# Kernel tuning notes

Hardware: AMD Instinct MI355X
Metric: run time of the kernel (lower is better)

## Reference

```python
import jax, jax.numpy as jnp
import numpy as np

H = 16
HIDDEN = 1024
B, S = 2, 2048


def setup_inputs() -> dict:
    key = jax.random.key(0)
    ks = jax.random.split(key, 6)
    return {
        "query": jax.random.normal(ks[0], (B, S, HIDDEN), dtype=jnp.float32),
        "key": jax.random.normal(ks[1], (B, S, HIDDEN), dtype=jnp.float32),
        "value": jax.random.normal(ks[2], (B, S, HIDDEN), dtype=jnp.float32),
        "W_query": jax.random.normal(ks[3], (HIDDEN, HIDDEN), dtype=jnp.float32) * 0.01,
        "W_key": jax.random.normal(ks[4], (HIDDEN, HIDDEN), dtype=jnp.float32) * 0.01,
        "W_value": jax.random.normal(ks[5], (HIDDEN, HIDDEN), dtype=jnp.float32) * 0.01,
        "ln_gamma": jnp.ones((HIDDEN,), dtype=jnp.float32),
        "ln_beta": jnp.zeros((HIDDEN,), dtype=jnp.float32),
        "mask": 1,
    }


def reference(query, key, value, W_query, W_key, W_value, ln_gamma, ln_beta, mask):
    b, s, hidden = query.shape
    d = hidden // H  # chunk_size per head
    # project then split last dim into heads, head axis leading: [h, b, s, d]
    def heads(x, W):
        return jnp.transpose((x @ W).reshape(b, s, H, d), (2, 0, 1, 3))
    q = heads(query, W_query)
    k = heads(key, W_key)
    v = heads(value, W_value)
    scale = jnp.asarray(np.sqrt(d), dtype=query.dtype)
    scores = jnp.einsum("hbqd,hbkd->hbqk", q, k) / scale
    aw = jax.nn.softmax(scores, axis=-1)
    if mask:
        tril = jnp.tril(jnp.ones((s, s), dtype=aw.dtype))  # post-softmax mask
        aw = aw * tril
        aw = aw / jnp.sum(aw, axis=3, keepdims=True)
    ws = jnp.einsum("hbqk,hbkd->hbqd", aw, v)
    # concat heads back on last dim: [b, s, hidden]
    ws = jnp.transpose(ws, (1, 2, 0, 3)).reshape(b, s, hidden)
    out = ws + query
    # LayerNorm over last dim, eps=1e-5 (torch default)
    mean = jnp.mean(out, axis=-1, keepdims=True)
    var = jnp.mean(jnp.square(out - mean), axis=-1, keepdims=True)
    out = (out - mean) / jnp.sqrt(var + 1e-5) * ln_gamma + ln_beta
    return out, aw
```

## Files before the change

### kernel.cpp

```cpp
#include <hip/hip_runtime.h>

typedef unsigned short ushort_t;
typedef __attribute__((ext_vector_type(4))) float f32x4;
typedef __attribute__((ext_vector_type(8))) short short8;
typedef __attribute__((ext_vector_type(8))) unsigned short ushort8;

#define B_DIM 2
#define S_LEN 2048
#define HID 1024
#define NH 16
#define HD 64
#define NROWS (B_DIM * S_LEN)

__device__ __forceinline__ ushort_t f2bf(float f) {
  union { float f; unsigned u; } v; v.f = f;
  unsigned r = v.u + 0x7FFFu + ((v.u >> 16) & 1u);
  return (ushort_t)(r >> 16);
}

__device__ __forceinline__ f32x4 zero4() {
  f32x4 z = {0.f, 0.f, 0.f, 0.f};
  return z;
}

struct WcArgs { const float* W[3]; ushort_t* T[3]; };

__global__ __launch_bounds__(256) void wconv_kernel(WcArgs args) {
  __shared__ ushort_t L[64 * 65];
  const int k0 = blockIdx.x * 64, n0 = blockIdx.y * 64;
  const float* __restrict__ W = args.W[blockIdx.z];
  ushort_t* __restrict__ T = args.T[blockIdx.z];
  const int tid = threadIdx.x;
  for (int i = 0; i < 4; ++i) {
    int idx = i * 256 + tid;
    int row = idx >> 4;
    int f4  = idx & 15;
    f32x4 v = *(const f32x4*)(W + (size_t)(k0 + row) * HID + n0 + f4 * 4);
    for (int j = 0; j < 4; ++j)
      L[(f4 * 4 + j) * 65 + row] = f2bf(v[j]);
  }
  __syncthreads();
  for (int i = 0; i < 2; ++i) {
    int idx = i * 256 + tid;
    int row = idx >> 3;
    int seg = idx & 7;
    ushort8 u;
    for (int j = 0; j < 8; ++j) u[j] = L[row * 65 + seg * 8 + j];
    *(ushort8*)(T + (size_t)(n0 + row) * HID + k0 + seg * 8) = u;
  }
}

struct PgArgs { const float* A[3]; const ushort_t* Wt[3]; ushort_t* C[3]; };

__global__ __launch_bounds__(256) void proj_gemm(PgArgs args) {
  __shared__ ushort_t As[128 * 64];
  __shared__ ushort_t Bs[128 * 64];
  const int z = blockIdx.z;
  const float* __restrict__ A = args.A[z];
  const ushort_t* __restrict__ Wt = args.Wt[z];
  ushort_t* __restrict__ C = args.C[z];
  const int tid = threadIdx.x;
  const int w = tid >> 6, lane = tid & 63, g = lane >> 4, c = lane & 15;
  const int wm = w >> 1, wn = w & 1;
  const int m0 = blockIdx.y * 128, n0 = blockIdx.x * 128;
  const int swz = (c & 7) << 3;

  f32x4 acc[4][4];
  for (int mi = 0; mi < 4; ++mi)
    for (int ni = 0; ni < 4; ++ni) acc[mi][ni] = zero4();

  for (int kt = 0; kt < 16; ++kt) {
    const int k0 = kt * 64;
    __syncthreads();
    for (int i = 0; i < 4; ++i) {
      int idx = i * 256 + tid;
      int row = idx >> 3, seg = idx & 7;
      const float* src = A + (size_t)(m0 + row) * HID + k0 + seg * 8;
      f32x4 a0 = *(const f32x4*)src;
      f32x4 a1 = *(const f32x4*)(src + 4);
      ushort8 u;
      u[0] = f2bf(a0[0]); u[1] = f2bf(a0[1]); u[2] = f2bf(a0[2]); u[3] = f2bf(a0[3]);
      u[4] = f2bf(a1[0]); u[5] = f2bf(a1[1]); u[6] = f2bf(a1[2]); u[7] = f2bf(a1[3]);
      *(ushort8*)&As[row * 64 + ((seg * 8) ^ ((row & 7) << 3))] = u;
    }
    for (int i = 0; i < 4; ++i) {
      int idx = i * 256 + tid;
      int row = idx >> 3, seg = idx & 7;
      ushort8 u = *(const ushort8*)(Wt + (size_t)(n0 + row) * HID + k0 + seg * 8);
      *(ushort8*)&Bs[row * 64 + ((seg * 8) ^ ((row & 7) << 3))] = u;
    }
    __syncthreads();
    for (int ks = 0; ks < 2; ++ks) {
      short8 af[4], bf4[4];
      for (int mi = 0; mi < 4; ++mi)
        af[mi] = *(const short8*)&As[(wm * 64 + mi * 16 + c) * 64 + ((ks * 32 + 8 * g) ^ swz)];
      for (int ni = 0; ni < 4; ++ni)
        bf4[ni] = *(const short8*)&Bs[(wn * 64 + ni * 16 + c) * 64 + ((ks * 32 + 8 * g) ^ swz)];
      for (int mi = 0; mi < 4; ++mi)
        for (int ni = 0; ni < 4; ++ni)
          acc[mi][ni] = __builtin_amdgcn_mfma_f32_16x16x32_bf16(af[mi], bf4[ni], acc[mi][ni], 0, 0, 0);
    }
  }
  for (int mi = 0; mi < 4; ++mi)
    for (int ni = 0; ni < 4; ++ni)
      for (int r = 0; r < 4; ++r)
        C[(size_t)(m0 + wm * 64 + mi * 16 + 4 * g + r) * HID + n0 + wn * 64 + ni * 16 + c] =
            f2bf(acc[mi][ni][r]);
}

__global__ __launch_bounds__(256) void attn_kernel(const ushort_t* __restrict__ Qb,
    const ushort_t* __restrict__ Kb, const ushort_t* __restrict__ Vb,
    float* __restrict__ aw, float* __restrict__ wsa) {
  __shared__ ushort_t Ks[64 * 64];
  __shared__ ushort_t Vt[64 * 64];
  __shared__ ushort_t Ps[4 * 16 * 64];

  const int tid = threadIdx.x;
  const int w = tid >> 6, lane = tid & 63, g = lane >> 4, c = lane & 15;
  const int qt = blockIdx.x, hb = blockIdx.y;
  const int h = hb >> 1, b = hb & 1;
  const int q0 = qt * 64;
  const int swz = (c & 7) << 3;
  const float C2 = 0.18033688011112042f;

  short8 aq[2];
  {
    const ushort_t* qp = Qb + (size_t)(b * S_LEN + q0 + w * 16 + c) * HID + h * HD + 8 * g;
    aq[0] = *(const short8*)qp;
    aq[1] = *(const short8*)(qp + 32);
  }

  float rs[4] = {0.f, 0.f, 0.f, 0.f};

  for (int kt = 0; kt <= qt; ++kt) {
    const int kc0 = kt * 64;
    __syncthreads();
    for (int i = 0; i < 2; ++i) {
      int idx = i * 256 + tid;
      int kk = idx >> 3, seg = idx & 7;
      const ushort_t* src = Kb + (size_t)(b * S_LEN + kc0 + kk) * HID + h * HD + seg * 8;
      *(ushort8*)&Ks[kk * 64 + ((seg * 8) ^ ((kk & 7) << 3))] = *(const ushort8*)src;
    }
    __syncthreads();
    f32x4 sf[4];
    for (int nf = 0; nf < 4; ++nf) sf[nf] = zero4();
    for (int ks = 0; ks < 2; ++ks) {
      short8 bk[4];
      for (int nf = 0; nf < 4; ++nf)
        bk[nf] = *(const short8*)&Ks[(nf * 16 + c) * 64 + ((ks * 32 + 8 * g) ^ swz)];
      for (int nf = 0; nf < 4; ++nf)
        sf[nf] = __builtin_amdgcn_mfma_f32_16x16x32_bf16(aq[ks], bk[nf], sf[nf], 0, 0, 0);
    }
    if (kt == qt) {
      for (int nf = 0; nf < 4; ++nf)
        for (int r = 0; r < 4; ++r)
          rs[r] += (nf * 16 + c > w * 16 + 4 * g + r) ? 0.f : exp2f(sf[nf][r] * C2);
    } else {
      for (int nf = 0; nf < 4; ++nf)
        for (int r = 0; r < 4; ++r) rs[r] += exp2f(sf[nf][r] * C2);
    }
  }
  for (int m = 1; m <= 8; m <<= 1)
    for (int r = 0; r < 4; ++r) rs[r] += __shfl_xor(rs[r], m);
  float linv[4];
  for (int r = 0; r < 4; ++r) linv[r] = 1.0f / rs[r];

  f32x4 oacc[4];
  for (int nf = 0; nf < 4; ++nf) oacc[nf] = zero4();

  for (int kt = 0; kt <= qt; ++kt) {
    const int kc0 = kt * 64;
    __syncthreads();
    for (int i = 0; i < 2; ++i) {
      int idx = i * 256 + tid;
      int kk = idx >> 3, seg = idx & 7;
      const ushort_t* src = Kb + (size_t)(b * S_LEN + kc0 + kk) * HID + h * HD + seg * 8;
      *(ushort8*)&Ks[kk * 64 + ((seg * 8) ^ ((kk & 7) << 3))] = *(const ushort8*)src;
    }
    for (int i = 0; i < 2; ++i) {
      int idx = i * 256 + tid;
      int dd = idx & 63, kseg = idx >> 6;
      ushort8 tv;
      for (int j = 0; j < 8; ++j)
        tv[j] = Vb[(size_t)(b * S_LEN + kc0 + kseg * 8 + j) * HID + h * HD + dd];
      *(ushort8*)&Vt[dd * 64 + ((kseg * 8) ^ ((dd & 7) << 3))] = tv;
    }
    __syncthreads();
    f32x4 sf[4];
    for (int nf = 0; nf < 4; ++nf) sf[nf] = zero4();
    for (int ks = 0; ks < 2; ++ks) {
      short8 bk[4];
      for (int nf = 0; nf < 4; ++nf)
        bk[nf] = *(const short8*)&Ks[(nf * 16 + c) * 64 + ((ks * 32 + 8 * g) ^ swz)];
      for (int nf = 0; nf < 4; ++nf)
        sf[nf] = __builtin_amdgcn_mfma_f32_16x16x32_bf16(aq[ks], bk[nf], sf[nf], 0, 0, 0);
    }
    const bool diag = (kt == qt);
    for (int nf = 0; nf < 4; ++nf) {
      for (int r = 0; r < 4; ++r) {
        float p = exp2f(sf[nf][r] * C2) * linv[r];
        if (diag && (nf * 16 + c > w * 16 + 4 * g + r)) p = 0.f;
        const int r16 = 4 * g + r;
        aw[((size_t)hb * S_LEN + q0 + w * 16 + r16) * S_LEN + kc0 + nf * 16 + c] = p;
        Ps[w * 1024 + r16 * 64 + ((nf * 16 + c) ^ ((r16 & 7) << 3))] = f2bf(p);
      }
    }
    for (int ks = 0; ks < 2; ++ks) {
      short8 pa = *(const short8*)&Ps[w * 1024 + c * 64 + ((ks * 32 + 8 * g) ^ swz)];
      short8 bv[4];
      for (int nf = 0; nf < 4; ++nf)
        bv[nf] = *(const short8*)&Vt[(nf * 16 + c) * 64 + ((ks * 32 + 8 * g) ^ swz)];
      for (int nf = 0; nf < 4; ++nf)
        oacc[nf] = __builtin_amdgcn_mfma_f32_16x16x32_bf16(pa, bv[nf], oacc[nf], 0, 0, 0);
    }
  }

  for (int nf = 0; nf < 4; ++nf)
    for (int r = 0; r < 4; ++r)
      wsa[(size_t)(b * S_LEN + q0 + w * 16 + 4 * g + r) * HID + h * HD + nf * 16 + c] =
          oacc[nf][r];

  const int z0 = (qt + 1) * 64;
  if (z0 < S_LEN) {
    const int row = tid >> 2, t4 = tid & 3;
    f32x4* rowp = (f32x4*)(aw + ((size_t)hb * S_LEN + q0 + row) * S_LEN);
    const f32x4 zz = zero4();
    for (int c4 = (z0 >> 2) + t4; c4 < (S_LEN >> 2); c4 += 4) rowp[c4] = zz;
  }
}

__global__ __launch_bounds__(256) void ln_kernel(const float* __restrict__ wsa,
    const float* __restrict__ qin, const float* __restrict__ gamma,
    const float* __restrict__ beta, float* __restrict__ out) {
  __shared__ float red[8];
  const int row = blockIdx.x, tid = threadIdx.x;
  const size_t base = (size_t)row * HID + tid * 4;
  f32x4 xv = *(const f32x4*)(wsa + base);
  f32x4 qv = *(const f32x4*)(qin + base);
  f32x4 x = xv + qv;
  float s = x[0] + x[1] + x[2] + x[3];
  float sq = x[0] * x[0] + x[1] * x[1] + x[2] * x[2] + x[3] * x[3];
  for (int m = 1; m <= 32; m <<= 1) {
    s += __shfl_xor(s, m);
    sq += __shfl_xor(sq, m);
  }
  if ((tid & 63) == 0) {
    red[(tid >> 6) * 2] = s;
    red[(tid >> 6) * 2 + 1] = sq;
  }
  __syncthreads();
  s = red[0] + red[2] + red[4] + red[6];
  sq = red[1] + red[3] + red[5] + red[7];
  const float mean = s * (1.0f / HID);
  const float var = sq * (1.0f / HID) - mean * mean;
  const float rstd = 1.0f / sqrtf(var + 1e-5f);
  f32x4 gm = *(const f32x4*)(gamma + tid * 4);
  f32x4 bt = *(const f32x4*)(beta + tid * 4);
  f32x4 o;
  for (int j = 0; j < 4; ++j) o[j] = (x[j] - mean) * rstd * gm[j] + bt[j];
  *(f32x4*)(out + base) = o;
}

extern "C" void kernel_launch(void* const* d_in, const int* in_sizes, int n_in,
                              void* d_out, int out_size, void* d_ws, size_t ws_size,
                              hipStream_t stream) {
  (void)in_sizes; (void)n_in; (void)out_size; (void)ws_size;
  const float* q_in = (const float*)d_in[0];
  const float* k_in = (const float*)d_in[1];
  const float* v_in = (const float*)d_in[2];
  const float* wq   = (const float*)d_in[3];
  const float* wk   = (const float*)d_in[4];
  const float* wv   = (const float*)d_in[5];
  const float* gamma = (const float*)d_in[6];
  const float* beta  = (const float*)d_in[7];

  ushort_t* base = (ushort_t*)d_ws;
  ushort_t* Wt0 = base;
  ushort_t* Wt1 = Wt0 + 1048576;
  ushort_t* Wt2 = Wt1 + 1048576;
  ushort_t* Qb = Wt2 + 1048576;
  ushort_t* Kb = Qb + 4194304;
  ushort_t* Vb = Kb + 4194304;
  float* wsa = (float*)(Vb + 4194304);

  float* out = (float*)d_out;
  float* aw = out + (size_t)NROWS * HID;

  WcArgs wc{{wq, wk, wv}, {Wt0, Wt1, Wt2}};
  wconv_kernel<<<dim3(16, 16, 3), 256, 0, stream>>>(wc);

  PgArgs pg{{q_in, k_in, v_in}, {Wt0, Wt1, Wt2}, {Qb, Kb, Vb}};
  proj_gemm<<<dim3(8, 32, 3), 256, 0, stream>>>(pg);

  attn_kernel<<<dim3(32, 32), 256, 0, stream>>>(Qb, Kb, Vb, aw, wsa);

  ln_kernel<<<dim3(NROWS), 256, 0, stream>>>(wsa, q_in, gamma, beta, out);
}
```

Before: 809.7 us.

## Pair causal query tiles per block, pre-transpose V, prefetch K/V, bf16 attention output

The attention kernel now gives each block a low and a high query tile (p and 31-p), which balances the causal work and lets both tiles share each loaded K/V tile. A separate kernel pre-transposes V so attention loads it with vector reads instead of strided scalar gathers. K/V tiles for the next step are prefetched into registers while the current one is computed, and QK^T is computed transposed so aw rows can be stored as vectors. The attention output is also stored as bf16 to cut LN input traffic, at some accuracy cost and with an extra kernel launch and more register pressure.

```diff
diff --git a/kernel.cpp b/kernel.cpp
--- a/kernel.cpp
+++ b/kernel.cpp
@@ -2,6 +2,7 @@
 
 typedef unsigned short ushort_t;
 typedef __attribute__((ext_vector_type(4))) float f32x4;
+typedef __attribute__((ext_vector_type(4))) unsigned short u16x4;
 typedef __attribute__((ext_vector_type(8))) short short8;
 typedef __attribute__((ext_vector_type(8))) unsigned short ushort8;
 
@@ -18,9 +19,21 @@
   return (ushort_t)(r >> 16);
 }
 
+__device__ __forceinline__ float bf2f(ushort_t h) {
+  union { unsigned u; float f; } v;
+  v.u = ((unsigned)h) << 16;
+  return v.f;
+}
+
 __device__ __forceinline__ f32x4 zero4() {
   f32x4 z = {0.f, 0.f, 0.f, 0.f};
   return z;
+}
+
+__device__ __forceinline__ unsigned pk2(float a, float b) {
+  unsigned r;
+  asm("v_cvt_pk_bf16_f32 %0, %1, %2" : "=v"(r) : "v"(a), "v"(b));
+  return r;
 }
 
 struct WcArgs { const float* W[3]; ushort_t* T[3]; };
@@ -108,136 +121,246 @@
             f2bf(acc[mi][ni][r]);
 }
 
+__global__ __launch_bounds__(256) void vtrans_kernel(const ushort_t* __restrict__ Vb,
+                                                     ushort_t* __restrict__ VT) {
+  __shared__ ushort_t L[64 * 72];
+  const int s0 = blockIdx.x * 64, hb = blockIdx.y;
+  const int h = hb >> 1, b = hb & 1;
+  const int tid = threadIdx.x;
+#pragma unroll
+  for (int i = 0; i < 2; ++i) {
+    int idx = i * 256 + tid;
+    int sr = idx >> 3, seg = idx & 7;
+    ushort8 u = *(const ushort8*)(Vb + ((size_t)(b * S_LEN) + s0 + sr) * HID + h * HD + seg * 8);
+    *(ushort8*)&L[sr * 72 + seg * 8] = u;
+  }
+  __syncthreads();
+#pragma unroll
+  for (int i = 0; i < 2; ++i) {
+    int idx = i * 256 + tid;
+    int d = idx >> 3, seg2 = idx & 7;
+    ushort8 u;
+#pragma unroll
+    for (int j = 0; j < 8; ++j) u[j] = L[(seg2 * 8 + j) * 72 + d];
+    *(ushort8*)(VT + ((size_t)hb * HD + d) * S_LEN + s0 + seg2 * 8) = u;
+  }
+}
+
+#define C2S 0.18033688011112042f
+
+__device__ __forceinline__ void qkt_tile(const ushort_t* Ks, int g, int c,
+                                         const short8 qB[2], f32x4 st[4]) {
+#pragma unroll
+  for (int nf = 0; nf < 4; ++nf) st[nf] = zero4();
+#pragma unroll
+  for (int ks = 0; ks < 2; ++ks) {
+#pragma unroll
+    for (int nf = 0; nf < 4; ++nf) {
+      short8 kf = *(const short8*)&Ks[(nf * 16 + c) * 64 + 8 * ((4 * ks + g) ^ (c & 7))];
+      st[nf] = __builtin_amdgcn_mfma_f32_16x16x32_bf16(kf, qB[ks], st[nf], 0, 0, 0);
+    }
+  }
+}
+
+__device__ __forceinline__ float tile_sum(const f32x4 st[4], int g, int c, int wq, bool diag) {
+  float s = 0.f;
+#pragma unroll
+  for (int nf = 0; nf < 4; ++nf)
+#pragma unroll
+    for (int r = 0; r < 4; ++r) {
+      float e = exp2f(st[nf][r] * C2S);
+      bool m = diag && (nf * 16 + 4 * g + r > wq);
+      s += m ? 0.f : e;
+    }
+  return s;
+}
+
+__device__ __forceinline__ void tile_p_pv(const f32x4 st[4], float linv, int g, int c,
+                                          bool diag, int wq, float* __restrict__ awrow,
+                                          char* psb, const short8 vf[2][4], f32x4 oacc[4]) {
+#pragma unroll
+  for (int nf = 0; nf < 4; ++nf) {
+    f32x4 pv;
+#pragma unroll
+    for (int r = 0; r < 4; ++r) {
+      float e = exp2f(st[nf][r] * C2S) * linv;
+      bool m = diag && (nf * 16 + 4 * g + r > wq);
+      pv[r] = m ? 0.f : e;
+    }
+    *(f32x4*)(awrow + nf * 16 + 4 * g) = pv;
+    uint2 u;
+    u.x = pk2(pv[0], pv[1]);
+    u.y = pk2(pv[2], pv[3]);
+    *(uint2*)(psb + (c * 128 + ((32 * nf + 8 * g) ^ ((c & 7) << 4)))) = u;
+  }
+#pragma unroll
+  for (int ks = 0; ks < 2; ++ks) {
+    short8 pf = *(const short8*)(psb + (c * 128 + ((64 * ks + 16 * g) ^ ((c & 7) << 4))));
+#pragma unroll
+    for (int nf = 0; nf < 4; ++nf)
+      oacc[nf] = __builtin_amdgcn_mfma_f32_16x16x32_bf16(vf[ks][nf], pf, oacc[nf], 0, 0, 0);
+  }
+}
+
 __global__ __launch_bounds__(256) void attn_kernel(const ushort_t* __restrict__ Qb,
-    const ushort_t* __restrict__ Kb, const ushort_t* __restrict__ Vb,
-    float* __restrict__ aw, float* __restrict__ wsa) {
+    const ushort_t* __restrict__ Kb, const ushort_t* __restrict__ VT,
+    float* __restrict__ aw, ushort_t* __restrict__ wsa) {
   __shared__ ushort_t Ks[64 * 64];
   __shared__ ushort_t Vt[64 * 64];
   __shared__ ushort_t Ps[4 * 16 * 64];
 
   const int tid = threadIdx.x;
   const int w = tid >> 6, lane = tid & 63, g = lane >> 4, c = lane & 15;
-  const int qt = blockIdx.x, hb = blockIdx.y;
+  const int p = blockIdx.x, hb = blockIdx.y;
   const int h = hb >> 1, b = hb & 1;
-  const int q0 = qt * 64;
-  const int swz = (c & 7) << 3;
-  const float C2 = 0.18033688011112042f;
-
-  short8 aq[2];
+  const int lo = p, hi = 31 - p;
+  const int wq = w * 16 + c;
+  const int srow = tid >> 3, sseg = tid & 7;
+
+  short8 qlo[2], qhi[2];
   {
-    const ushort_t* qp = Qb + (size_t)(b * S_LEN + q0 + w * 16 + c) * HID + h * HD + 8 * g;
-    aq[0] = *(const short8*)qp;
-    aq[1] = *(const short8*)(qp + 32);
-  }
-
-  float rs[4] = {0.f, 0.f, 0.f, 0.f};
-
-  for (int kt = 0; kt <= qt; ++kt) {
+    const ushort_t* qp = Qb + ((size_t)(b * S_LEN) + lo * 64 + wq) * HID + h * HD + 8 * g;
+    qlo[0] = *(const short8*)qp;
+    qlo[1] = *(const short8*)(qp + 32);
+    const ushort_t* qp2 = Qb + ((size_t)(b * S_LEN) + hi * 64 + wq) * HID + h * HD + 8 * g;
+    qhi[0] = *(const short8*)qp2;
+    qhi[1] = *(const short8*)(qp2 + 32);
+  }
+
+  ushort8 kr[2], vr[2], kn[2], vn[2];
+
+#pragma unroll
+  for (int i = 0; i < 2; ++i) {
+    int row = i * 32 + srow;
+    kr[i] = *(const ushort8*)(Kb + ((size_t)(b * S_LEN) + row) * HID + h * HD + sseg * 8);
+  }
+#pragma unroll
+  for (int i = 0; i < 2; ++i) {
+    int row = i * 32 + srow;
+    *(ushort8*)&Ks[row * 64 + 8 * (sseg ^ (row & 7))] = kr[i];
+  }
+  __syncthreads();
+
+  float ps_lo = 0.f, ps_hi = 0.f;
+  for (int kt = 0; kt <= hi; ++kt) {
+    if (kt < hi) {
+#pragma unroll
+      for (int i = 0; i < 2; ++i) {
+        int row = i * 32 + srow;
+        kn[i] = *(const ushort8*)(Kb + ((size_t)(b * S_LEN) + (kt + 1) * 64 + row) * HID + h * HD + sseg * 8);
+      }
+    }
+    f32x4 st[4];
+    qkt_tile(Ks, g, c, qhi, st);
+    ps_hi += tile_sum(st, g, c, wq, kt == hi);
+    if (kt <= lo) {
+      qkt_tile(Ks, g, c, qlo, st);
+      ps_lo += tile_sum(st, g, c, wq, kt == lo);
+    }
+    __syncthreads();
+    if (kt < hi) {
+#pragma unroll
+      for (int i = 0; i < 2; ++i) {
+        int row = i * 32 + srow;
+        *(ushort8*)&Ks[row * 64 + 8 * (sseg ^ (row & 7))] = kn[i];
+      }
+    }
+    __syncthreads();
+  }
+  ps_lo += __shfl_xor(ps_lo, 16); ps_lo += __shfl_xor(ps_lo, 32);
+  ps_hi += __shfl_xor(ps_hi, 16); ps_hi += __shfl_xor(ps_hi, 32);
+  const float linv_lo = 1.0f / ps_lo, linv_hi = 1.0f / ps_hi;
+
+  f32x4 oLo[4], oHi[4];
+#pragma unroll
+  for (int nf = 0; nf < 4; ++nf) { oLo[nf] = zero4(); oHi[nf] = zero4(); }
+
+#pragma unroll
+  for (int i = 0; i < 2; ++i) {
+    int row = i * 32 + srow;
+    kr[i] = *(const ushort8*)(Kb + ((size_t)(b * S_LEN) + row) * HID + h * HD + sseg * 8);
+    vr[i] = *(const ushort8*)(VT + ((size_t)hb * HD + row) * S_LEN + sseg * 8);
+  }
+#pragma unroll
+  for (int i = 0; i < 2; ++i) {
+    int row = i * 32 + srow;
+    *(ushort8*)&Ks[row * 64 + 8 * (sseg ^ (row & 7))] = kr[i];
+    *(ushort8*)&Vt[row * 64 + 8 * (sseg ^ (row & 7))] = vr[i];
+  }
+  __syncthreads();
+
+  char* psb = (char*)Ps + w * 2048;
+  for (int kt = 0; kt <= hi; ++kt) {
     const int kc0 = kt * 64;
-    __syncthreads();
-    for (int i = 0; i < 2; ++i) {
-      int idx = i * 256 + tid;
-      int kk = idx >> 3, seg = idx & 7;
-      const ushort_t* src = Kb + (size_t)(b * S_LEN + kc0 + kk) * HID + h * HD + seg * 8;
-      *(ushort8*)&Ks[kk * 64 + ((seg * 8) ^ ((kk & 7) << 3))] = *(const ushort8*)src;
-    }
-    __syncthreads();
-    f32x4 sf[4];
-    for (int nf = 0; nf < 4; ++nf) sf[nf] = zero4();
-    for (int ks = 0; ks < 2; ++ks) {
-      short8 bk[4];
+    if (kt < hi) {
+#pragma unroll
+      for (int i = 0; i < 2; ++i) {
+        int row = i * 32 + srow;
+        kn[i] = *(const ushort8*)(Kb + ((size_t)(b * S_LEN) + kc0 + 64 + row) * HID + h * HD + sseg * 8);
+        vn[i] = *(const ushort8*)(VT + ((size_t)hb * HD + row) * S_LEN + kc0 + 64 + sseg * 8);
+      }
+    }
+    short8 vf[2][4];
+#pragma unroll
+    for (int ks = 0; ks < 2; ++ks)
+#pragma unroll
       for (int nf = 0; nf < 4; ++nf)
-        bk[nf] = *(const short8*)&Ks[(nf * 16 + c) * 64 + ((ks * 32 + 8 * g) ^ swz)];
-      for (int nf = 0; nf < 4; ++nf)
-        sf[nf] = __builtin_amdgcn_mfma_f32_16x16x32_bf16(aq[ks], bk[nf], sf[nf], 0, 0, 0);
-    }
-    if (kt == qt) {
-      for (int nf = 0; nf < 4; ++nf)
-        for (int r = 0; r < 4; ++r)
-          rs[r] += (nf * 16 + c > w * 16 + 4 * g + r) ? 0.f : exp2f(sf[nf][r] * C2);
-    } else {
-      for (int nf = 0; nf < 4; ++nf)
-        for (int r = 0; r < 4; ++r) rs[r] += exp2f(sf[nf][r] * C2);
-    }
-  }
-  for (int m = 1; m <= 8; m <<= 1)
-    for (int r = 0; r < 4; ++r) rs[r] += __shfl_xor(rs[r], m);
-  float linv[4];
-  for (int r = 0; r < 4; ++r) linv[r] = 1.0f / rs[r];
-
-  f32x4 oacc[4];
-  for (int nf = 0; nf < 4; ++nf) oacc[nf] = zero4();
-
-  for (int kt = 0; kt <= qt; ++kt) {
-    const int kc0 = kt * 64;
-    __syncthreads();
-    for (int i = 0; i < 2; ++i) {
-      int idx = i * 256 + tid;
-      int kk = idx >> 3, seg = idx & 7;
-      const ushort_t* src = Kb + (size_t)(b * S_LEN + kc0 + kk) * HID + h * HD + seg * 8;
-      *(ushort8*)&Ks[kk * 64 + ((seg * 8) ^ ((kk & 7) << 3))] = *(const ushort8*)src;
-    }
-    for (int i = 0; i < 2; ++i) {
-      int idx = i * 256 + tid;
-      int dd = idx & 63, kseg = idx >> 6;
-      ushort8 tv;
-      for (int j = 0; j < 8; ++j)
-        tv[j] = Vb[(size_t)(b * S_LEN + kc0 + kseg * 8 + j) * HID + h * HD + dd];
-      *(ushort8*)&Vt[dd * 64 + ((kseg * 8) ^ ((dd & 7) << 3))] = tv;
-    }
-    __syncthreads();
-    f32x4 sf[4];
-    for (int nf = 0; nf < 4; ++nf) sf[nf] = zero4();
-    for (int ks = 0; ks < 2; ++ks) {
-      short8 bk[4];
-      for (int nf = 0; nf < 4; ++nf)
-        bk[nf] = *(const short8*)&Ks[(nf * 16 + c) * 64 + ((ks * 32 + 8 * g) ^ swz)];
-      for (int nf = 0; nf < 4; ++nf)
-        sf[nf] = __builtin_amdgcn_mfma_f32_16x16x32_bf16(aq[ks], bk[nf], sf[nf], 0, 0, 0);
-    }
-    const bool diag = (kt == qt);
-    for (int nf = 0; nf < 4; ++nf) {
-      for (int r = 0; r < 4; ++r) {
-        float p = exp2f(sf[nf][r] * C2) * linv[r];
-        if (diag && (nf * 16 + c > w * 16 + 4 * g + r)) p = 0.f;
-        const int r16 = 4 * g + r;
-        aw[((size_t)hb * S_LEN + q0 + w * 16 + r16) * S_LEN + kc0 + nf * 16 + c] = p;
-        Ps[w * 1024 + r16 * 64 + ((nf * 16 + c) ^ ((r16 & 7) << 3))] = f2bf(p);
+        vf[ks][nf] = *(const short8*)&Vt[(nf * 16 + c) * 64 + 8 * ((4 * ks + g) ^ (c & 7))];
+
+    f32x4 st[4];
+    qkt_tile(Ks, g, c, qhi, st);
+    {
+      float* awrow = aw + ((size_t)hb * S_LEN + hi * 64 + wq) * S_LEN + kc0;
+      tile_p_pv(st, linv_hi, g, c, kt == hi, wq, awrow, psb, vf, oHi);
+    }
+    if (kt <= lo) {
+      qkt_tile(Ks, g, c, qlo, st);
+      float* awrow = aw + ((size_t)hb * S_LEN + lo * 64 + wq) * S_LEN + kc0;
+      tile_p_pv(st, linv_lo, g, c, kt == lo, wq, awrow, psb, vf, oLo);
+    }
+    __syncthreads();
+    if (kt < hi) {
+#pragma unroll
+      for (int i = 0; i < 2; ++i) {
+        int row = i * 32 + srow;
+        *(ushort8*)&Ks[row * 64 + 8 * (sseg ^ (row & 7))] = kn[i];
+        *(ushort8*)&Vt[row * 64 + 8 * (sseg ^ (row & 7))] = vn[i];
       }
     }
-    for (int ks = 0; ks < 2; ++ks) {
-      short8 pa = *(const short8*)&Ps[w * 1024 + c * 64 + ((ks * 32 + 8 * g) ^ swz)];
-      short8 bv[4];
-      for (int nf = 0; nf < 4; ++nf)
-        bv[nf] = *(const short8*)&Vt[(nf * 16 + c) * 64 + ((ks * 32 + 8 * g) ^ swz)];
-      for (int nf = 0; nf < 4; ++nf)
-        oacc[nf] = __builtin_amdgcn_mfma_f32_16x16x32_bf16(pa, bv[nf], oacc[nf], 0, 0, 0);
-    }
-  }
-
-  for (int nf = 0; nf < 4; ++nf)
-    for (int r = 0; r < 4; ++r)
-      wsa[(size_t)(b * S_LEN + q0 + w * 16 + 4 * g + r) * HID + h * HD + nf * 16 + c] =
-          oacc[nf][r];
-
-  const int z0 = (qt + 1) * 64;
-  if (z0 < S_LEN) {
-    const int row = tid >> 2, t4 = tid & 3;
-    f32x4* rowp = (f32x4*)(aw + ((size_t)hb * S_LEN + q0 + row) * S_LEN);
-    const f32x4 zz = zero4();
-    for (int c4 = (z0 >> 2) + t4; c4 < (S_LEN >> 2); c4 += 4) rowp[c4] = zz;
-  }
-}
-
-__global__ __launch_bounds__(256) void ln_kernel(const float* __restrict__ wsa,
+    __syncthreads();
+  }
+
+#pragma unroll
+  for (int nf = 0; nf < 4; ++nf) {
+    uint2 uh, ul;
+    uh.x = pk2(oHi[nf][0], oHi[nf][1]); uh.y = pk2(oHi[nf][2], oHi[nf][3]);
+    ul.x = pk2(oLo[nf][0], oLo[nf][1]); ul.y = pk2(oLo[nf][2], oLo[nf][3]);
+    *(uint2*)(wsa + ((size_t)(b * S_LEN) + hi * 64 + wq) * HID + h * HD + nf * 16 + 4 * g) = uh;
+    *(uint2*)(wsa + ((size_t)(b * S_LEN) + lo * 64 + wq) * HID + h * HD + nf * 16 + 4 * g) = ul;
+  }
+
+  const f32x4 zz = zero4();
+#pragma unroll
+  for (int t = 0; t < 2; ++t) {
+    const int tIdx = t ? hi : lo;
+    const int z0q = (tIdx + 1) * 16;
+    for (int rr = 0; rr < 16; ++rr) {
+      f32x4* rowp = (f32x4*)(aw + ((size_t)hb * S_LEN + tIdx * 64 + w * 16 + rr) * S_LEN);
+      for (int c4 = z0q + lane; c4 < 512; c4 += 64) rowp[c4] = zz;
+    }
+  }
+}
+
+__global__ __launch_bounds__(256) void ln_kernel(const ushort_t* __restrict__ wsa,
     const float* __restrict__ qin, const float* __restrict__ gamma,
     const float* __restrict__ beta, float* __restrict__ out) {
   __shared__ float red[8];
   const int row = blockIdx.x, tid = threadIdx.x;
   const size_t base = (size_t)row * HID + tid * 4;
-  f32x4 xv = *(const f32x4*)(wsa + base);
+  u16x4 xh = *(const u16x4*)(wsa + base);
   f32x4 qv = *(const f32x4*)(qin + base);
-  f32x4 x = xv + qv;
+  f32x4 x;
+  for (int j = 0; j < 4; ++j) x[j] = bf2f(xh[j]) + qv[j];
   float s = x[0] + x[1] + x[2] + x[3];
   float sq = x[0] * x[0] + x[1] * x[1] + x[2] * x[2] + x[3] * x[3];
   for (int m = 1; m <= 32; m <<= 1) {
@@ -281,7 +404,8 @@
   ushort_t* Qb = Wt2 + 1048576;
   ushort_t* Kb = Qb + 4194304;
   ushort_t* Vb = Kb + 4194304;
-  float* wsa = (float*)(Vb + 4194304);
+  ushort_t* VT = Vb + 4194304;
+  ushort_t* wsa = VT + 4194304;
 
   float* out = (float*)d_out;
   float* aw = out + (size_t)NROWS * HID;
@@ -292,7 +416,9 @@
   PgArgs pg{{q_in, k_in, v_in}, {Wt0, Wt1, Wt2}, {Qb, Kb, Vb}};
   proj_gemm<<<dim3(8, 32, 3), 256, 0, stream>>>(pg);
 
-  attn_kernel<<<dim3(32, 32), 256, 0, stream>>>(Qb, Kb, Vb, aw, wsa);
+  vtrans_kernel<<<dim3(32, 32), 256, 0, stream>>>(Vb, VT);
+
+  attn_kernel<<<dim3(16, 32), 256, 0, stream>>>(Qb, Kb, VT, aw, wsa);
 
   ln_kernel<<<dim3(NROWS), 256, 0, stream>>>(wsa, q_in, gamma, beta, out);
 }
```

Result: faster. 725.2 us (-10.4%).
